# Kernel optimization log

Hardware: AMD Instinct MI355X
Metric: run time of the kernel (lower is better)

The kernel has to match this reference:

```python
import jax, jax.numpy as jnp
import numpy as np

B, GL, GF, N = 4, 4, 128, 1024
CS, CN, NA = 32, 16, 16
S, HS = 512, 512


def squash(s, axis):
    # mag_sq/(1+mag_sq) * s/mag == s * mag/(1+mag_sq)
    mag_sq = jnp.sum(s * s, axis=axis, keepdims=True)
    return s * (jnp.sqrt(mag_sq) / (1.0 + mag_sq))


def routing(u_hat, n_iter=3):
    # u_hat: [M, I, J, U]; dynamic routing, softmax over J, squash over J (as in source)
    M, I, J, U = u_hat.shape
    b = jnp.zeros((I, J), dtype=u_hat.dtype)
    v = None
    for _ in range(n_iter):
        c = jax.nn.softmax(b, axis=1)                       # [I, J]
        s = jnp.einsum('ij,miju->mju', c, u_hat)            # [M, J, U]
        v = squash(s, axis=1)                               # squash over J (torch dim=2)
        b = b + jnp.einsum('miju,mju->mij', u_hat, v).mean(axis=0)
    return v


def setup_inputs():
    key = jax.random.key(0)
    ks = jax.random.split(key, 7)
    sc = 0.1
    return {
        'graph_embed': jax.random.normal(ks[0], (B, GL, GF, N), jnp.float32),
        'hidden': jax.random.normal(ks[1], (B, S, HS), jnp.float32),
        'Wp': jax.random.normal(ks[2], (GL, CS, GL, GF), jnp.float32) * sc,  # per-unit conv kernels
        'bp': jax.random.normal(ks[3], (GL, CS), jnp.float32) * sc,
        'Wg': jax.random.normal(ks[4], (CS, CN, CS, GL), jnp.float32) * sc,  # graph caps [I,J,U,K]
        'Wa': jax.random.normal(ks[5], (CS + HS,), jnp.float32) * sc,        # attention_1 weight
        'Ws': jax.random.normal(ks[6], (CN, NA, CS, CS), jnp.float32) * sc,  # aspect caps [I,J,U,K]
    }


def _per_example(x, h, Wp, bp, Wg, Wa, Ws):
    # x: [GL, GF, N], h: [S, HS]
    gl, gf, n = x.shape
    # primary capsules: each unit's conv kernel covers all (GL,GF) -> full contraction
    u = jnp.einsum('uclf,lfn->ucn', Wp, x) + bp[:, :, None]   # [GL, CS, N]
    u = squash(u.reshape(gl, -1), axis=1)                     # squash over CS*N (torch dim=2)
    p = u.reshape(n, gl, CS)                                  # torch .view(-1, GL, CS)
    # graph capsule routing
    u_hat_g = jnp.einsum('ijuk,mik->miju', Wg, p.transpose(0, 2, 1))  # [N, CS, CN, CS]
    v_g = routing(u_hat_g)                                    # [N, CN, CS]
    g = v_g.reshape(n, CS, CN).mean(axis=0).reshape(CN, CS)   # torch .view semantics
    # adaptive attention: Linear([g;h]) with no bias, softmax over capsules
    score = jax.nn.softmax((g @ Wa[:CS])[None, :] + (h @ Wa[CS:])[:, None], axis=1)  # [S, CN]
    condensed = g[None, :, :] * score[:, :, None]             # [S, CN, CS]
    # aspect capsule routing (transpose(1,2) then layer-internal transpose cancel out)
    u_hat_a = jnp.einsum('ijuk,mik->miju', Ws, condensed)     # [S, CN, NA, CS]
    return routing(u_hat_a)                                   # [S, NA, CS]


def reference(graph_embed, hidden, Wp, bp, Wg, Wa, Ws):
    f = jax.vmap(_per_example, in_axes=(0, 0, None, None, None, None, None))
    return f(graph_embed, hidden, Wp, bp, Wg, Wa, Ws)   # [B, S, NA, CS]
```

## Files before the change

### kernel.cpp

```cpp
#include <hip/hip_runtime.h>
#include <math.h>


static constexpr int OFF_U  = 0;
static constexpr int OFF_S  = 524288;
static constexpr int OFF_SS = 2621440;
static constexpr int OFF_BG = 2621456;
static constexpr int OFF_G  = 2623504;
static constexpr int OFF_VA = 2625552;
static constexpr int OFF_MS = 2627600;
static constexpr int OFF_UH = 2758672;

__global__ void k_primary_part(const float* __restrict__ X, const float* __restrict__ Wp,
                               float* __restrict__ Upart)
{
    __shared__ float Wt[128 * 68];
    const int ct = blockIdx.x, nt = blockIdx.y;
    const int b = blockIdx.z >> 2, ks = blockIdx.z & 3;
    const int t = threadIdx.x;
    const int tn = t & 15, tc = t >> 4;
    const int c0 = ct * 64, n0 = nt * 64;
#pragma unroll
    for (int i = 0; i < 8; ++i) {
        const int idx = t + i * 256;
        const int c = idx >> 5, k4 = idx & 31;
        const float4 wv = *(const float4*)&Wp[(size_t)(c0 + c) * 512 + ks * 128 + k4 * 4];
        Wt[(k4 * 4 + 0) * 68 + c] = wv.x;
        Wt[(k4 * 4 + 1) * 68 + c] = wv.y;
        Wt[(k4 * 4 + 2) * 68 + c] = wv.z;
        Wt[(k4 * 4 + 3) * 68 + c] = wv.w;
    }
    __syncthreads();
    float acc[4][4] = {};
    const float* Xp = X + (size_t)b * 524288 + (size_t)(ks * 128) * 1024 + n0 + tn * 4;
#pragma unroll 4
    for (int k = 0; k < 128; ++k) {
        const float4 xv = *(const float4*)(Xp + (size_t)k * 1024);
        const float4 wv = *(const float4*)&Wt[k * 68 + tc * 4];
        const float w[4] = {wv.x, wv.y, wv.z, wv.w};
        const float x[4] = {xv.x, xv.y, xv.z, xv.w};
#pragma unroll
        for (int ci = 0; ci < 4; ++ci)
#pragma unroll
            for (int ni = 0; ni < 4; ++ni)
                acc[ci][ni] = fmaf(w[ci], x[ni], acc[ci][ni]);
    }
    float* up = Upart + (size_t)ks * 524288 + (size_t)b * 131072;
#pragma unroll
    for (int ci = 0; ci < 4; ++ci)
        *(float4*)&up[(size_t)(c0 + tc * 4 + ci) * 1024 + n0 + tn * 4] =
            make_float4(acc[ci][0], acc[ci][1], acc[ci][2], acc[ci][3]);
}

__global__ void k_reduceU(const float* __restrict__ Upart, const float* __restrict__ bp,
                          float* __restrict__ U, float* __restrict__ SS)
{
    __shared__ float red[256];
    const int blk = blockIdx.x, t = threadIdx.x;
    const int b = blk >> 5, cg = blk & 31;
    float ssq = 0.f;
#pragma unroll
    for (int i = 0; i < 4; ++i) {
        const int c = cg * 4 + i;
        const int f4 = b * 32768 + c * 256 + t;
        float4 s = ((const float4*)Upart)[f4];
#pragma unroll
        for (int ks = 1; ks < 4; ++ks) {
            const float4 p = ((const float4*)Upart)[ks * 131072 + f4];
            s.x += p.x; s.y += p.y; s.z += p.z; s.w += p.w;
        }
        const float bv = bp[c];
        s.x += bv; s.y += bv; s.z += bv; s.w += bv;
        ssq = fmaf(s.x, s.x, ssq); ssq = fmaf(s.y, s.y, ssq);
        ssq = fmaf(s.z, s.z, ssq); ssq = fmaf(s.w, s.w, ssq);
        ((float4*)U)[f4] = s;
    }
    red[t] = ssq;
    __syncthreads();
    for (int s = 128; s > 0; s >>= 1) {
        if (t < s) red[t] += red[t + s];
        __syncthreads();
    }
    if (t == 0) atomicAdd(&SS[b * 4 + (cg >> 3)], red[0]);
}

__global__ void k_smatmul(const float* __restrict__ U, const float* __restrict__ SS,
                          const float* __restrict__ Bg, const float* __restrict__ Wg,
                          float* __restrict__ S)
{
    __shared__ __align__(16) float Pt[64 * 68];
    __shared__ __align__(16) float Ct[64 * 68];
    __shared__ float cls[512];
    const int mt = blockIdx.x, jt = blockIdx.y, b = blockIdx.z;
    const int t = threadIdx.x;
    const int tj = t & 15, tm = t >> 4;
    if (t < 32) {
        float vals[16];
        float mx = -1e30f;
        for (int j = 0; j < 16; ++j) { vals[j] = Bg[b * 512 + t * 16 + j]; mx = fmaxf(mx, vals[j]); }
        float sum = 0.f;
        for (int j = 0; j < 16; ++j) { vals[j] = expf(vals[j] - mx); sum += vals[j]; }
        const float inv = 1.f / sum;
        for (int j = 0; j < 16; ++j) cls[t * 16 + j] = vals[j] * inv;
    }
    const float ss = SS[b * 4 + (mt >> 2)];
    const float sc = sqrtf(ss) / (1.f + ss);
    float acc[4][4] = {};
    const float* Ub = U + (size_t)b * 131072 + (size_t)mt * 64 * 128;
    __syncthreads();
    for (int kc = 0; kc < 2; ++kc) {
        for (int x = t; x < 64 * 64; x += 256) {
            const int r = x >> 6, cq = x & 63;
            Pt[r * 68 + cq] = Ub[r * 128 + kc * 64 + cq] * sc;
            const int q = kc * 64 + cq;
            const int i = q & 31, kk = q >> 5;
            const int ju = jt * 64 + r;
            const int j = ju >> 5, u = ju & 31;
            Ct[r * 68 + cq] = cls[i * 16 + j] * Wg[((i * 16 + j) * 32 + u) * 4 + kk];
        }
        __syncthreads();
#pragma unroll 4
        for (int q0 = 0; q0 < 64; q0 += 4) {
            float4 pa[4], cb[4];
#pragma unroll
            for (int mm = 0; mm < 4; ++mm)
                pa[mm] = *(const float4*)&Pt[(tm * 4 + mm) * 68 + q0];
#pragma unroll
            for (int jj = 0; jj < 4; ++jj)
                cb[jj] = *(const float4*)&Ct[(tj + 16 * jj) * 68 + q0];
#pragma unroll
            for (int mm = 0; mm < 4; ++mm) {
#pragma unroll
                for (int jj = 0; jj < 4; ++jj) {
                    acc[mm][jj] = fmaf(pa[mm].x, cb[jj].x, acc[mm][jj]);
                    acc[mm][jj] = fmaf(pa[mm].y, cb[jj].y, acc[mm][jj]);
                    acc[mm][jj] = fmaf(pa[mm].z, cb[jj].z, acc[mm][jj]);
                    acc[mm][jj] = fmaf(pa[mm].w, cb[jj].w, acc[mm][jj]);
                }
            }
        }
        __syncthreads();
    }
#pragma unroll
    for (int mm = 0; mm < 4; ++mm) {
        float* Sp = S + (size_t)b * 524288 + (size_t)(mt * 64 + tm * 4 + mm) * 512
                      + jt * 64 + tj;
#pragma unroll
        for (int jj = 0; jj < 4; ++jj)
            Sp[jj * 16] = acc[mm][jj];
    }
}

__global__ void k_mag(const float* __restrict__ S, float* __restrict__ MS)
{
    const int t = threadIdx.x;
    const int u = t & 31, ml = t >> 5;
    const int m = blockIdx.x * 8 + ml;
    const int b = blockIdx.y;
    const float* row = S + (size_t)b * 524288 + (size_t)m * 512;
    float mag = 0.f;
#pragma unroll
    for (int j = 0; j < 16; ++j) { const float v = row[j * 32 + u]; mag = fmaf(v, v, mag); }
    MS[b * 32768 + m * 32 + u] = sqrtf(mag) / (1.f + mag);
}

__global__ void k_maggmean(const float* __restrict__ S, float* __restrict__ G)
{
    __shared__ float gacc[512];
    const int t = threadIdx.x;
    gacc[t] = 0.f; gacc[t + 256] = 0.f;
    const int u = t & 31, mlg = t >> 5;
    const int b = blockIdx.y;
    const int m0 = blockIdx.x * 32 + mlg * 4;
    float preg[16];
#pragma unroll
    for (int j = 0; j < 16; ++j) preg[j] = 0.f;
    __syncthreads();
#pragma unroll
    for (int mi = 0; mi < 4; ++mi) {
        const float* row = S + (size_t)b * 524288 + (size_t)(m0 + mi) * 512;
        float sv[16];
        float mag = 0.f;
#pragma unroll
        for (int j = 0; j < 16; ++j) { sv[j] = row[j * 32 + u]; mag = fmaf(sv[j], sv[j], mag); }
        const float msc = sqrtf(mag) / (1.f + mag);
#pragma unroll
        for (int j = 0; j < 16; ++j) preg[j] = fmaf(sv[j], msc, preg[j]);
    }
#pragma unroll
    for (int j = 0; j < 16; ++j) atomicAdd(&gacc[j * 32 + u], preg[j]);
    __syncthreads();
    atomicAdd(&G[b * 512 + t], gacc[t] * (1.f / 1024.f));
    atomicAdd(&G[b * 512 + 256 + t], gacc[t + 256] * (1.f / 1024.f));
}

__global__ void k_tbu(const float* __restrict__ U, const float* __restrict__ SS,
                      const float* __restrict__ S, const float* __restrict__ MS,
                      const float* __restrict__ Wg, float* __restrict__ Bg)
{
    __shared__ float Ps[64 * 132];
    __shared__ float Vs[64 * 68];
    __shared__ float bup[64];
    const int jt = blockIdx.x, mc = blockIdx.y, b = blockIdx.z;
    const int t = threadIdx.x;
    const int tq = t & 31, tjv = t >> 5;
    const int m0 = mc * 64;
    if (t < 64) bup[t] = 0.f;
    const float ss = SS[b * 4 + (mc >> 2)];
    const float sc = sqrtf(ss) / (1.f + ss);
#pragma unroll
    for (int i = 0; i < 8; ++i) {
        const int f4 = t + i * 256;
        const int r = f4 >> 5, q4 = f4 & 31;
        float4 v = *(const float4*)&U[(size_t)b * 131072 + (size_t)(m0 + r) * 128 + q4 * 4];
        v.x *= sc; v.y *= sc; v.z *= sc; v.w *= sc;
        *(float4*)&Ps[r * 132 + q4 * 4] = v;
    }
#pragma unroll
    for (int i = 0; i < 4; ++i) {
        const int f4 = t + i * 256;
        const int r = f4 >> 4, c4 = f4 & 15;
        const int m = m0 + r;
        float4 v = *(const float4*)&S[(size_t)b * 524288 + (size_t)m * 512 + jt * 64 + c4 * 4];
        const int ub = (c4 * 4) & 31;
        const float* msp = MS + b * 32768 + m * 32;
        v.x *= msp[ub + 0]; v.y *= msp[ub + 1]; v.z *= msp[ub + 2]; v.w *= msp[ub + 3];
        *(float4*)&Vs[r * 68 + c4 * 4] = v;
    }
    __syncthreads();
    float acc[4][8] = {};
#pragma unroll 2
    for (int m = 0; m < 64; ++m) {
        const float4 p4 = *(const float4*)&Ps[m * 132 + tq * 4];
        const float4 va = *(const float4*)&Vs[m * 68 + tjv * 8];
        const float4 vb = *(const float4*)&Vs[m * 68 + tjv * 8 + 4];
        const float pv[4] = {p4.x, p4.y, p4.z, p4.w};
        const float vv[8] = {va.x, va.y, va.z, va.w, vb.x, vb.y, vb.z, vb.w};
#pragma unroll
        for (int qi = 0; qi < 4; ++qi)
#pragma unroll
            for (int ji = 0; ji < 8; ++ji)
                acc[qi][ji] = fmaf(pv[qi], vv[ji], acc[qi][ji]);
    }
    const int k = tq >> 3;
    const int j_loc = tjv >> 2;
    const int j = jt * 2 + j_loc;
    const int u0 = (tjv & 3) * 8;
#pragma unroll
    for (int qi = 0; qi < 4; ++qi) {
        const int i = (tq & 7) * 4 + qi;
        const float* wp = Wg + ((i * 16 + j) * 32) * 4 + k;
        float s = 0.f;
#pragma unroll
        for (int ji = 0; ji < 8; ++ji)
            s = fmaf(wp[(u0 + ji) * 4], acc[qi][ji], s);
        s += __shfl_xor(s, 8);
        s += __shfl_xor(s, 16);
        s += __shfl_xor(s, 32);
        if ((t & 56) == 0) atomicAdd(&bup[i * 2 + j_loc], s);
    }
    __syncthreads();
    if (t < 64) {
        const int ii = t >> 1, jl = t & 1;
        atomicAdd(&Bg[b * 512 + ii * 16 + jt * 2 + jl], bup[t] * (1.f / 1024.f));
    }
}

__global__ void k_uhat(const float* __restrict__ G, const float* __restrict__ Wa,
                       const float* __restrict__ Ws, float* __restrict__ UH)
{
    const int b = blockIdx.y;
    const int t = threadIdx.x;
    __shared__ float g[512], cond[512], score[16], red[16];
    g[t] = G[b * 512 + t];
    g[t + 256] = G[b * 512 + 256 + t];
    __syncthreads();
    if (t < 16) {
        float s = 0.f;
        for (int u = 0; u < 32; ++u) s = fmaf(g[t * 32 + u], Wa[u], s);
        red[t] = s;
    }
    __syncthreads();
    if (t == 0) {
        float mx = -1e30f;
        for (int j = 0; j < 16; ++j) mx = fmaxf(mx, red[j]);
        float sum = 0.f;
        for (int j = 0; j < 16; ++j) { score[j] = expf(red[j] - mx); sum += score[j]; }
        const float inv = 1.f / sum;
        for (int j = 0; j < 16; ++j) score[j] *= inv;
    }
    __syncthreads();
    cond[t] = g[t] * score[t >> 5];
    cond[t + 256] = g[t + 256] * score[(t + 256) >> 5];
    __syncthreads();
    const int e0 = blockIdx.x * 1024 + t * 4;
    const int i = e0 >> 9;
    const float* cp = cond + i * 32;
    const float* wp = Ws + (size_t)e0 * 32;
    float res[4];
#pragma unroll
    for (int jj = 0; jj < 4; ++jj) {
        float s = 0.f;
#pragma unroll
        for (int k8 = 0; k8 < 8; ++k8) {
            const float4 w = *(const float4*)(wp + jj * 32 + k8 * 4);
            s = fmaf(w.x, cp[k8 * 4 + 0], s);
            s = fmaf(w.y, cp[k8 * 4 + 1], s);
            s = fmaf(w.z, cp[k8 * 4 + 2], s);
            s = fmaf(w.w, cp[k8 * 4 + 3], s);
        }
        res[jj] = s;
    }
    ((float4*)UH)[(b * 8192 + e0) >> 2] = make_float4(res[0], res[1], res[2], res[3]);
}

__global__ void k_route(const float* __restrict__ UH, float* __restrict__ VA)
{
    const int b = blockIdx.x;
    const int t = threadIdx.x;
    __shared__ float uh[8192], ba[256], cc[256], sbuf[512], msc[32];
#pragma unroll
    for (int i = 0; i < 8; ++i)
        ((float4*)uh)[i * 256 + t] = ((const float4*)UH)[b * 2048 + i * 256 + t];
    ba[t] = 0.f;
    __syncthreads();
    for (int it = 0; it < 3; ++it) {
        if (t < 16) {
            float mx = -1e30f;
            for (int j = 0; j < 16; ++j) mx = fmaxf(mx, ba[t * 16 + j]);
            float sum = 0.f;
            for (int j = 0; j < 16; ++j) { cc[t * 16 + j] = expf(ba[t * 16 + j] - mx); sum += cc[t * 16 + j]; }
            const float inv = 1.f / sum;
            for (int j = 0; j < 16; ++j) cc[t * 16 + j] *= inv;
        }
        __syncthreads();
        for (int h = 0; h < 2; ++h) {
            const int e = h * 256 + t;
            const int j = e >> 5;
            float s = 0.f;
            for (int i = 0; i < 16; ++i) s = fmaf(cc[i * 16 + j], uh[i * 512 + e], s);
            sbuf[e] = s;
        }
        __syncthreads();
        if (t < 32) {
            float mg = 0.f;
            for (int j = 0; j < 16; ++j) { const float x = sbuf[j * 32 + t]; mg = fmaf(x, x, mg); }
            msc[t] = sqrtf(mg) / (1.f + mg);
        }
        __syncthreads();
        for (int h = 0; h < 2; ++h) {
            const int e = h * 256 + t;
            sbuf[e] *= msc[e & 31];
        }
        __syncthreads();
        if (it < 2) {
            const int i = t >> 4, j = t & 15;
            float s = 0.f;
            for (int u = 0; u < 32; ++u) s = fmaf(uh[i * 512 + j * 32 + u], sbuf[j * 32 + u], s);
            ba[t] += s;
            __syncthreads();
        }
    }
    VA[b * 512 + t] = sbuf[t];
    VA[b * 512 + 256 + t] = sbuf[256 + t];
}

__global__ void k_out(const float* __restrict__ VA, float* __restrict__ out)
{
    const int idx = blockIdx.x * 256 + threadIdx.x;
    const int b = idx >> 16;
    const int jv4 = idx & 127;
    ((float4*)out)[idx] = ((const float4*)VA)[b * 128 + jv4];
}

extern "C" void kernel_launch(void* const* d_in, const int* in_sizes, int n_in,
                              void* d_out, int out_size, void* d_ws, size_t ws_size,
                              hipStream_t stream)
{
    const float* X   = (const float*)d_in[0];
    const float* Wp  = (const float*)d_in[2];
    const float* bp  = (const float*)d_in[3];
    const float* Wg  = (const float*)d_in[4];
    const float* Wa  = (const float*)d_in[5];
    const float* Wsp = (const float*)d_in[6];
    float* out = (float*)d_out;
    float* ws = (float*)d_ws;

    float* U  = ws + OFF_U;
    float* S  = ws + OFF_S;
    float* SS = ws + OFF_SS;
    float* Bg = ws + OFF_BG;
    float* G  = ws + OFF_G;
    float* VA = ws + OFF_VA;
    float* MS = ws + OFF_MS;
    float* UH = ws + OFF_UH;

    hipMemsetAsync(SS, 0, (16 + 2048 + 2048) * sizeof(float), stream);

    k_primary_part<<<dim3(2, 16, 16), 256, 0, stream>>>(X, Wp, S);
    k_reduceU<<<128, 256, 0, stream>>>(S, bp, U, SS);

    for (int it = 0; it < 3; ++it) {
        k_smatmul<<<dim3(16, 8, 4), 256, 0, stream>>>(U, SS, Bg, Wg, S);
        if (it < 2) {
            k_mag<<<dim3(128, 4), 256, 0, stream>>>(S, MS);
            k_tbu<<<dim3(8, 16, 4), 256, 0, stream>>>(U, SS, S, MS, Wg, Bg);
        } else {
            k_maggmean<<<dim3(32, 4), 256, 0, stream>>>(S, G);
        }
    }

    k_uhat<<<dim3(8, 4), 256, 0, stream>>>(G, Wa, Wsp, UH);
    k_route<<<4, 256, 0, stream>>>(UH, VA);
    k_out<<<1024, 256, 0, stream>>>(VA, out);
}
```

Measured before the change: 227.3 us.

## Fuse squash magnitude and mean into routing matmul with pre-permuted Wg

The routing s-matmul now tiles over u-slices, so each block holds all 16 J values for 8 u's. That lets it compute the squash magnitude (MS) or the final mean into G in its epilogue, which removes the separate k_mag and k_maggmean launches and their re-read of S. Wg is permuted once into a coalesced layout by extra blocks added to the primary-conv launch, replacing the strided gather in the matmul tile load. The trade-off is a larger shared-memory tile, more accumulators per thread, and fewer blocks (256 instead of 512).

```diff
diff --git a/kernel.cpp b/kernel.cpp
--- a/kernel.cpp
+++ b/kernel.cpp
@@ -2,22 +2,36 @@
 #include <math.h>
 
 
-static constexpr int OFF_U  = 0;
-static constexpr int OFF_S  = 524288;
-static constexpr int OFF_SS = 2621440;
-static constexpr int OFF_BG = 2621456;
-static constexpr int OFF_G  = 2623504;
-static constexpr int OFF_VA = 2625552;
-static constexpr int OFF_MS = 2627600;
-static constexpr int OFF_UH = 2758672;
+static constexpr int OFF_U   = 0;
+static constexpr int OFF_S   = 524288;
+static constexpr int OFF_SS  = 2621440;
+static constexpr int OFF_BG  = 2621456;
+static constexpr int OFF_G   = 2623504;
+static constexpr int OFF_VA  = 2625552;
+static constexpr int OFF_MS  = 2627600;
+static constexpr int OFF_UH  = 2758672;
+static constexpr int OFF_WGR = 2791440;
 
 __global__ void k_primary_part(const float* __restrict__ X, const float* __restrict__ Wp,
-                               float* __restrict__ Upart)
+                               float* __restrict__ Upart,
+                               const float* __restrict__ Wg, float* __restrict__ Wgr)
 {
     __shared__ float Wt[128 * 68];
+    const int t = threadIdx.x;
+    if (blockIdx.z == 16) {
+        const int blk = blockIdx.x * 16 + blockIdx.y;
+#pragma unroll
+        for (int r = 0; r < 8; ++r) {
+            const int e = blk * 2048 + r * 256 + t;
+            const int q = e >> 9, rem = e & 511;
+            const int u = rem >> 4, j = rem & 15;
+            const int i = q & 31, kk = q >> 5;
+            Wgr[e] = Wg[((i * 16 + j) * 32 + u) * 4 + kk];
+        }
+        return;
+    }
     const int ct = blockIdx.x, nt = blockIdx.y;
     const int b = blockIdx.z >> 2, ks = blockIdx.z & 3;
-    const int t = threadIdx.x;
     const int tn = t & 15, tc = t >> 4;
     const int c0 = ct * 64, n0 = nt * 64;
 #pragma unroll
@@ -84,16 +98,21 @@
     if (t == 0) atomicAdd(&SS[b * 4 + (cg >> 3)], red[0]);
 }
 
-__global__ void k_smatmul(const float* __restrict__ U, const float* __restrict__ SS,
-                          const float* __restrict__ Bg, const float* __restrict__ Wg,
-                          float* __restrict__ S)
+__global__ __launch_bounds__(256) void k_smatmulM(
+    const float* __restrict__ U, const float* __restrict__ SS,
+    const float* __restrict__ Bg, const float* __restrict__ Wgr,
+    float* __restrict__ S, float* __restrict__ MS, float* __restrict__ G)
 {
     __shared__ __align__(16) float Pt[64 * 68];
-    __shared__ __align__(16) float Ct[64 * 68];
+    __shared__ __align__(16) float Ct[64 * 160];
     __shared__ float cls[512];
-    const int mt = blockIdx.x, jt = blockIdx.y, b = blockIdx.z;
+    __shared__ float gacc[128];
+    const int mt = blockIdx.x, us = blockIdx.y, b = blockIdx.z;
     const int t = threadIdx.x;
-    const int tj = t & 15, tm = t >> 4;
+    const int tm = t >> 4;
+    const int uu = t & 7, jh = (t >> 3) & 1;
+    const int m0 = mt * 64;
+
     if (t < 32) {
         float vals[16];
         float mx = -1e30f;
@@ -103,95 +122,98 @@
         const float inv = 1.f / sum;
         for (int j = 0; j < 16; ++j) cls[t * 16 + j] = vals[j] * inv;
     }
+    if (G != nullptr && t < 128) gacc[t] = 0.f;
     const float ss = SS[b * 4 + (mt >> 2)];
     const float sc = sqrtf(ss) / (1.f + ss);
-    float acc[4][4] = {};
-    const float* Ub = U + (size_t)b * 131072 + (size_t)mt * 64 * 128;
-    __syncthreads();
+    float acc[4][8] = {};
+    const float* Ub = U + (size_t)b * 131072 + (size_t)m0 * 128;
+    __syncthreads();
+
     for (int kc = 0; kc < 2; ++kc) {
-        for (int x = t; x < 64 * 64; x += 256) {
-            const int r = x >> 6, cq = x & 63;
-            Pt[r * 68 + cq] = Ub[r * 128 + kc * 64 + cq] * sc;
-            const int q = kc * 64 + cq;
-            const int i = q & 31, kk = q >> 5;
-            const int ju = jt * 64 + r;
-            const int j = ju >> 5, u = ju & 31;
-            Ct[r * 68 + cq] = cls[i * 16 + j] * Wg[((i * 16 + j) * 32 + u) * 4 + kk];
-        }
-        __syncthreads();
+#pragma unroll
+        for (int it = 0; it < 4; ++it) {
+            const int x = t + it * 256;
+            const int m = x & 63, q4 = x >> 6;
+            const float4 v = *(const float4*)&Ub[(size_t)m * 128 + kc * 64 + q4 * 4];
+            Pt[(q4 * 4 + 0) * 68 + m] = v.x * sc;
+            Pt[(q4 * 4 + 1) * 68 + m] = v.y * sc;
+            Pt[(q4 * 4 + 2) * 68 + m] = v.z * sc;
+            Pt[(q4 * 4 + 3) * 68 + m] = v.w * sc;
+        }
+#pragma unroll
+        for (int it = 0; it < 8; ++it) {
+            const int x = t + it * 256;
+            const int c4 = (x & 31) * 4, qL = x >> 5;
+            const int q = kc * 64 + qL;
+            const int i = q & 31;
+            const int j0 = c4 & 15;
+            const float4 w = *(const float4*)&Wgr[(size_t)q * 512 + us * 128 + c4];
+            const int cp = qL * 160 + c4 + ((c4 >> 4) << 2);
+            Ct[cp + 0] = cls[i * 16 + j0 + 0] * w.x;
+            Ct[cp + 1] = cls[i * 16 + j0 + 1] * w.y;
+            Ct[cp + 2] = cls[i * 16 + j0 + 2] * w.z;
+            Ct[cp + 3] = cls[i * 16 + j0 + 3] * w.w;
+        }
+        __syncthreads();
+        const int cbase = uu * 20 + jh * 8;
 #pragma unroll 4
-        for (int q0 = 0; q0 < 64; q0 += 4) {
-            float4 pa[4], cb[4];
+        for (int qL = 0; qL < 64; ++qL) {
+            const float4 p4 = *(const float4*)&Pt[qL * 68 + tm * 4];
+            const float4 ca = *(const float4*)&Ct[qL * 160 + cbase];
+            const float4 cb = *(const float4*)&Ct[qL * 160 + cbase + 4];
+            const float pm[4] = {p4.x, p4.y, p4.z, p4.w};
+            const float cj[8] = {ca.x, ca.y, ca.z, ca.w, cb.x, cb.y, cb.z, cb.w};
 #pragma unroll
             for (int mm = 0; mm < 4; ++mm)
-                pa[mm] = *(const float4*)&Pt[(tm * 4 + mm) * 68 + q0];
-#pragma unroll
-            for (int jj = 0; jj < 4; ++jj)
-                cb[jj] = *(const float4*)&Ct[(tj + 16 * jj) * 68 + q0];
-#pragma unroll
-            for (int mm = 0; mm < 4; ++mm) {
-#pragma unroll
-                for (int jj = 0; jj < 4; ++jj) {
-                    acc[mm][jj] = fmaf(pa[mm].x, cb[jj].x, acc[mm][jj]);
-                    acc[mm][jj] = fmaf(pa[mm].y, cb[jj].y, acc[mm][jj]);
-                    acc[mm][jj] = fmaf(pa[mm].z, cb[jj].z, acc[mm][jj]);
-                    acc[mm][jj] = fmaf(pa[mm].w, cb[jj].w, acc[mm][jj]);
-                }
-            }
-        }
-        __syncthreads();
-    }
+#pragma unroll
+                for (int jj = 0; jj < 8; ++jj)
+                    acc[mm][jj] = fmaf(pm[mm], cj[jj], acc[mm][jj]);
+        }
+        __syncthreads();
+    }
+
 #pragma unroll
     for (int mm = 0; mm < 4; ++mm) {
-        float* Sp = S + (size_t)b * 524288 + (size_t)(mt * 64 + tm * 4 + mm) * 512
-                      + jt * 64 + tj;
-#pragma unroll
-        for (int jj = 0; jj < 4; ++jj)
-            Sp[jj * 16] = acc[mm][jj];
-    }
-}
-
-__global__ void k_mag(const float* __restrict__ S, float* __restrict__ MS)
-{
-    const int t = threadIdx.x;
-    const int u = t & 31, ml = t >> 5;
-    const int m = blockIdx.x * 8 + ml;
-    const int b = blockIdx.y;
-    const float* row = S + (size_t)b * 524288 + (size_t)m * 512;
-    float mag = 0.f;
-#pragma unroll
-    for (int j = 0; j < 16; ++j) { const float v = row[j * 32 + u]; mag = fmaf(v, v, mag); }
-    MS[b * 32768 + m * 32 + u] = sqrtf(mag) / (1.f + mag);
-}
-
-__global__ void k_maggmean(const float* __restrict__ S, float* __restrict__ G)
-{
-    __shared__ float gacc[512];
-    const int t = threadIdx.x;
-    gacc[t] = 0.f; gacc[t + 256] = 0.f;
-    const int u = t & 31, mlg = t >> 5;
-    const int b = blockIdx.y;
-    const int m0 = blockIdx.x * 32 + mlg * 4;
-    float preg[16];
-#pragma unroll
-    for (int j = 0; j < 16; ++j) preg[j] = 0.f;
-    __syncthreads();
-#pragma unroll
-    for (int mi = 0; mi < 4; ++mi) {
-        const float* row = S + (size_t)b * 524288 + (size_t)(m0 + mi) * 512;
-        float sv[16];
-        float mag = 0.f;
-#pragma unroll
-        for (int j = 0; j < 16; ++j) { sv[j] = row[j * 32 + u]; mag = fmaf(sv[j], sv[j], mag); }
-        const float msc = sqrtf(mag) / (1.f + mag);
-#pragma unroll
-        for (int j = 0; j < 16; ++j) preg[j] = fmaf(sv[j], msc, preg[j]);
-    }
-#pragma unroll
-    for (int j = 0; j < 16; ++j) atomicAdd(&gacc[j * 32 + u], preg[j]);
-    __syncthreads();
-    atomicAdd(&G[b * 512 + t], gacc[t] * (1.f / 1024.f));
-    atomicAdd(&G[b * 512 + 256 + t], gacc[t + 256] * (1.f / 1024.f));
+        float* Sp = S + (size_t)b * 524288 + (size_t)(m0 + tm * 4 + mm) * 512 + us * 8 + uu;
+#pragma unroll
+        for (int jj = 0; jj < 8; ++jj)
+            Sp[(jh * 8 + jj) * 32] = acc[mm][jj];
+    }
+
+    if (G == nullptr) {
+#pragma unroll
+        for (int mm = 0; mm < 4; ++mm) {
+            float msq = 0.f;
+#pragma unroll
+            for (int jj = 0; jj < 8; ++jj) msq = fmaf(acc[mm][jj], acc[mm][jj], msq);
+            msq += __shfl_xor(msq, 8);
+            if (jh == 0)
+                MS[b * 32768 + (m0 + tm * 4 + mm) * 32 + us * 8 + uu] =
+                    sqrtf(msq) / (1.f + msq);
+        }
+    } else {
+        float part[8];
+#pragma unroll
+        for (int jj = 0; jj < 8; ++jj) part[jj] = 0.f;
+#pragma unroll
+        for (int mm = 0; mm < 4; ++mm) {
+            float msq = 0.f;
+#pragma unroll
+            for (int jj = 0; jj < 8; ++jj) msq = fmaf(acc[mm][jj], acc[mm][jj], msq);
+            msq += __shfl_xor(msq, 8);
+            const float msc = sqrtf(msq) / (1.f + msq);
+#pragma unroll
+            for (int jj = 0; jj < 8; ++jj) part[jj] = fmaf(acc[mm][jj], msc, part[jj]);
+        }
+#pragma unroll
+        for (int jj = 0; jj < 8; ++jj)
+            atomicAdd(&gacc[(jh * 8 + jj) * 8 + uu], part[jj]);
+        __syncthreads();
+        if (t < 128) {
+            const int j = t >> 3, u2 = t & 7;
+            atomicAdd(&G[b * 512 + j * 32 + us * 8 + u2], gacc[t] * (1.f / 1024.f));
+        }
+    }
 }
 
 __global__ void k_tbu(const float* __restrict__ U, const float* __restrict__ SS,
@@ -386,29 +408,26 @@
     float* out = (float*)d_out;
     float* ws = (float*)d_ws;
 
-    float* U  = ws + OFF_U;
-    float* S  = ws + OFF_S;
-    float* SS = ws + OFF_SS;
-    float* Bg = ws + OFF_BG;
-    float* G  = ws + OFF_G;
-    float* VA = ws + OFF_VA;
-    float* MS = ws + OFF_MS;
-    float* UH = ws + OFF_UH;
+    float* U   = ws + OFF_U;
+    float* S   = ws + OFF_S;
+    float* SS  = ws + OFF_SS;
+    float* Bg  = ws + OFF_BG;
+    float* G   = ws + OFF_G;
+    float* VA  = ws + OFF_VA;
+    float* MS  = ws + OFF_MS;
+    float* UH  = ws + OFF_UH;
+    float* Wgr = ws + OFF_WGR;
 
     hipMemsetAsync(SS, 0, (16 + 2048 + 2048) * sizeof(float), stream);
 
-    k_primary_part<<<dim3(2, 16, 16), 256, 0, stream>>>(X, Wp, S);
+    k_primary_part<<<dim3(2, 16, 17), 256, 0, stream>>>(X, Wp, S, Wg, Wgr);
     k_reduceU<<<128, 256, 0, stream>>>(S, bp, U, SS);
 
-    for (int it = 0; it < 3; ++it) {
-        k_smatmul<<<dim3(16, 8, 4), 256, 0, stream>>>(U, SS, Bg, Wg, S);
-        if (it < 2) {
-            k_mag<<<dim3(128, 4), 256, 0, stream>>>(S, MS);
-            k_tbu<<<dim3(8, 16, 4), 256, 0, stream>>>(U, SS, S, MS, Wg, Bg);
-        } else {
-            k_maggmean<<<dim3(32, 4), 256, 0, stream>>>(S, G);
-        }
-    }
+    k_smatmulM<<<dim3(16, 4, 4), 256, 0, stream>>>(U, SS, Bg, Wgr, S, MS, nullptr);
+    k_tbu<<<dim3(8, 16, 4), 256, 0, stream>>>(U, SS, S, MS, Wg, Bg);
+    k_smatmulM<<<dim3(16, 4, 4), 256, 0, stream>>>(U, SS, Bg, Wgr, S, MS, nullptr);
+    k_tbu<<<dim3(8, 16, 4), 256, 0, stream>>>(U, SS, S, MS, Wg, Bg);
+    k_smatmulM<<<dim3(16, 4, 4), 256, 0, stream>>>(U, SS, Bg, Wgr, S, nullptr, G);
 
     k_uhat<<<dim3(8, 4), 256, 0, stream>>>(G, Wa, Wsp, UH);
     k_route<<<4, 256, 0, stream>>>(UH, VA);
```

Measured after the change: 196.4 us. 1.16x faster.
